# Optimization experiments

Hardware: AMD Instinct MI355X
Metric: run time of the kernel (lower is better)

Reference implementation:

```python
import jax, jax.numpy as jnp
import numpy as np

N_ATOMS = 4096
N_EDGES = 131072
NUM_BASIS = 8
CUTOFF = 6.0
EMBED = 64      # atom embedding dim
HID = 128       # hidden channel width
SH_DIM = 9      # l=0,1,2 spherical harmonics
TP_IN = HID * SH_DIM  # 1152
N_HEADS = 4
HEAD_DIM = HID // N_HEADS


def _spherical_harmonics(vec):
    # vec: [E,3] -> [E,9] matching the torch SphericalHarmonics (l=0,1,2)
    r = jnp.linalg.norm(vec, axis=-1, keepdims=True) + 1e-8
    u = vec / r
    x, y, z = u[:, 0], u[:, 1], u[:, 2]
    l0 = jnp.ones_like(x)[:, None]
    l1 = jnp.stack([y, z, x], axis=-1)
    l2 = jnp.stack([3.0 * z * z - 1.0, x * z, y * z, x * y, x * x - y * y], axis=-1)
    return jnp.concatenate([l0, l1, l2], axis=-1)


def _rbf(d):
    # bessel RBF with cosine cutoff, d: [E] -> [E, NUM_BASIS]
    freqs = jnp.arange(1, NUM_BASIS + 1, dtype=d.dtype) * (np.pi / CUTOFF)
    cut = 0.5 * (jnp.cos(d * (np.pi / CUTOFF)) + 1.0) * (d < CUTOFF).astype(d.dtype)
    rbf = jnp.sin(d[:, None] * freqs) / d[:, None]
    return rbf * cut[:, None]


def _mace_block(atomic_numbers, edge_index, edge_vectors, edge_lengths,
                atom_embed, rad_w1, rad_b1, rad_w2, rad_b2, tp_w, tp_b,
                msg_w1, msg_b1, msg_w2, msg_b2,
                attn_w_in, attn_b_in, attn_w_out, attn_b_out,
                gate_w, gate_b, out_w, out_b):
    n_atoms = atom_embed.shape[0] if False else atomic_numbers.shape[0]
    node = atom_embed[atomic_numbers]                      # [N,64] gather
    sh = _spherical_harmonics(edge_vectors)                # [E,9]
    rbf = _rbf(edge_lengths)                               # [E,8]
    rad = jax.nn.silu(rbf @ rad_w1 + rad_b1)
    rad = jax.nn.silu(rad @ rad_w2 + rad_b2)               # [E,128]
    # per-l outer products radial x sh_l, flattened channel-major, concatenated
    slices = [(0, 1), (1, 4), (4, 9)]
    msgs = jnp.concatenate(
        [(rad[:, :, None] * sh[:, None, s:e]).reshape(rad.shape[0], -1) for s, e in slices],
        axis=-1)                                           # [E,1152]
    edge_msg = msgs @ tp_w + tp_b                          # [E,128]
    dst = edge_index[1]
    agg = jax.ops.segment_sum(edge_msg, dst, num_segments=n_atoms)  # [N,128] scatter-add
    combined = jnp.concatenate([node, agg], axis=-1)       # [N,192]
    upd = jax.nn.silu(combined @ msg_w1 + msg_b1) @ msg_w2 + msg_b2  # [N,128]
    # multi-head self-attention over all atoms (batch of 1)
    qkv = upd @ attn_w_in.T + attn_b_in                    # [N,384]
    q, k, v = jnp.split(qkv, 3, axis=-1)
    q = q.reshape(-1, N_HEADS, HEAD_DIM)
    k = k.reshape(-1, N_HEADS, HEAD_DIM)
    v = v.reshape(-1, N_HEADS, HEAD_DIM)
    scores = jnp.einsum('nhd,mhd->hnm', q, k) / np.sqrt(HEAD_DIM)
    attn = jax.nn.softmax(scores, axis=-1)
    att = jnp.einsum('hnm,mhd->nhd', attn, v).reshape(-1, HID)
    att = att @ attn_w_out.T + attn_b_out                  # [N,128]
    gate = jax.nn.sigmoid(upd @ gate_w + gate_b)
    out = gate * att + (1.0 - gate) * upd
    return out @ out_w + out_b                             # [N,128]


def setup_inputs() -> dict:
    key = jax.random.key(0)
    ks = jax.random.split(key, 20)
    def w(k, shape, s=0.05):
        return jax.random.normal(k, shape, dtype=jnp.float32) * s
    return {
        'atomic_numbers': jax.random.randint(ks[0], (N_ATOMS,), 0, 100),
        'positions': jax.random.normal(ks[1], (N_ATOMS, 3), dtype=jnp.float32),
        'edge_index': jax.random.randint(ks[2], (2, N_EDGES), 0, N_ATOMS),
        'edge_vectors': jax.random.normal(ks[3], (N_EDGES, 3), dtype=jnp.float32),
        'edge_lengths': jax.random.uniform(ks[4], (N_EDGES,), dtype=jnp.float32, minval=0.5, maxval=5.9),
        'atom_embed': w(ks[5], (100, EMBED), 1.0),
        'rad_w1': w(ks[6], (NUM_BASIS, 64)), 'rad_b1': jnp.zeros((64,), jnp.float32),
        'rad_w2': w(ks[7], (64, HID)), 'rad_b2': jnp.zeros((HID,), jnp.float32),
        'tp_w': w(ks[8], (TP_IN, HID)), 'tp_b': jnp.zeros((HID,), jnp.float32),
        'msg_w1': w(ks[9], (EMBED + HID, HID)), 'msg_b1': jnp.zeros((HID,), jnp.float32),
        'msg_w2': w(ks[10], (HID, HID)), 'msg_b2': jnp.zeros((HID,), jnp.float32),
        'attn_w_in': w(ks[11], (3 * HID, HID)), 'attn_b_in': jnp.zeros((3 * HID,), jnp.float32),
        'attn_w_out': w(ks[12], (HID, HID)), 'attn_b_out': jnp.zeros((HID,), jnp.float32),
        'gate_w': w(ks[13], (HID, HID)), 'gate_b': jnp.zeros((HID,), jnp.float32),
        'out_w': w(ks[14], (HID, HID)), 'out_b': jnp.zeros((HID,), jnp.float32),
    }


def reference(atomic_numbers, positions, edge_index, edge_vectors, edge_lengths,
              atom_embed, rad_w1, rad_b1, rad_w2, rad_b2, tp_w, tp_b,
              msg_w1, msg_b1, msg_w2, msg_b2,
              attn_w_in, attn_b_in, attn_w_out, attn_b_out,
              gate_w, gate_b, out_w, out_b):
    # positions is accepted (as in the torch signature) but unused by the block math
    del positions
    return _mace_block(atomic_numbers, edge_index, edge_vectors, edge_lengths,
                       atom_embed, rad_w1, rad_b1, rad_w2, rad_b2, tp_w, tp_b,
                       msg_w1, msg_b1, msg_w2, msg_b2,
                       attn_w_in, attn_b_in, attn_w_out, attn_b_out,
                       gate_w, gate_b, out_w, out_b)
```

## Files before the change

kernel.cpp:

```cpp
#include <hip/hip_runtime.h>
#include <math.h>

#define N_ATOMS 4096
#define N_EDGES 131072
#define PI6 0.52359877559829887f
#define CAP 128

typedef __attribute__((ext_vector_type(8))) short bf16x8;
typedef __attribute__((ext_vector_type(4))) float f32x4;

#define MFMA(A,B,C) __builtin_amdgcn_mfma_f32_16x16x32_bf16((A),(B),(C),0,0,0)

__device__ __forceinline__ float silu_f(float x){ return x / (1.f + __expf(-x)); }
__device__ __forceinline__ float sigmoid_f(float x){ return 1.f / (1.f + __expf(-x)); }
__device__ __forceinline__ unsigned int f2bf(float f){
  unsigned int u = __float_as_uint(f);
  return (u + 0x7FFFu + ((u>>16)&1u)) >> 16;
}
__device__ __forceinline__ bf16x8 ld8(const unsigned short* p){
  union { unsigned int u[4]; bf16x8 v; } r;
  const unsigned int* q = (const unsigned int*)p;
  r.u[0]=q[0]; r.u[1]=q[1]; r.u[2]=q[2]; r.u[3]=q[3];
  return r.v;
}
__device__ __forceinline__ void split_store(float v, unsigned short* ph, unsigned short* pl){
  unsigned int hb = f2bf(v);
  *ph = (unsigned short)hb;
  *pl = (unsigned short)f2bf(v - __uint_as_float(hb<<16));
}

__global__ __launch_bounds__(256) void prep_kernel(
  const float* __restrict__ attn_w_out, const float* __restrict__ rad_w2,
  const float* __restrict__ tp_w, const float* __restrict__ msg_w1,
  const float* __restrict__ msg_w2, const float* __restrict__ attn_w_in,
  float* __restrict__ wt_out, int* __restrict__ cursor,
  unsigned short* __restrict__ w2t_h, unsigned short* __restrict__ w2t_l,
  unsigned short* __restrict__ tpwT_h, unsigned short* __restrict__ tpwT_l,
  unsigned short* __restrict__ w1T_h, unsigned short* __restrict__ w1T_l,
  unsigned short* __restrict__ w2T_h, unsigned short* __restrict__ w2T_l,
  unsigned short* __restrict__ awin_h, unsigned short* __restrict__ awin_l)
{
  int idx = blockIdx.x*256 + threadIdx.x;
  if (idx < 4096) cursor[idx] = 0;
  if (idx < 16384){
    int i = idx>>7, k = idx&127;
    wt_out[k*128+i] = attn_w_out[idx];
  } else if (idx < 24576){
    int j = idx - 16384; int k = j>>7, c = j&127;
    split_store(rad_w2[k*128+c], &w2t_h[c*64+k], &w2t_l[c*64+k]);
  } else if (idx < 172032){
    int j = idx - 24576; int col = j&127, kk = j>>7;
    int jj = kk>>7, c = kk&127;
    int r = (jj==0)? c : (jj<4 ? 128 + c*3 + (jj-1) : 512 + c*5 + (jj-4));
    split_store(tp_w[r*128+col], &tpwT_h[col*1152+kk], &tpwT_l[col*1152+kk]);
  } else if (idx < 196608){
    int j = idx - 172032; int col = j&127, k = j>>7;
    split_store(msg_w1[k*128+col], &w1T_h[col*192+k], &w1T_l[col*192+k]);
  } else if (idx < 212992){
    int j = idx - 196608; int col = j&127, k = j>>7;
    split_store(msg_w2[k*128+col], &w2T_h[col*128+k], &w2T_l[col*128+k]);
  } else if (idx < 262144){
    int j = idx - 212992;
    split_store(attn_w_in[j], &awin_h[j], &awin_l[j]);
  }
}

__global__ __launch_bounds__(256) void bucket_kernel(
  const int* __restrict__ edge_index, int* __restrict__ cursor, int* __restrict__ edge_slot)
{
  int e = blockIdx.x*256 + threadIdx.x;
  if (e < N_EDGES){
    int d = edge_index[N_EDGES + e];
    int pos = atomicAdd(&cursor[d], 1);
    if (pos < CAP) edge_slot[d*CAP + pos] = e;
  }
}

__global__ __launch_bounds__(512) void edge_F_kernel(
  const float* __restrict__ edge_vectors, const float* __restrict__ edge_lengths,
  const float* __restrict__ rad_w1, const float* __restrict__ rad_b1,
  const unsigned short* __restrict__ w2t_h, const unsigned short* __restrict__ w2t_l,
  const float* __restrict__ rad_b2,
  const int* __restrict__ cursor, const int* __restrict__ edge_slot,
  unsigned short* __restrict__ Fh, unsigned short* __restrict__ Fl)
{
  const int tid = threadIdx.x;
  const int w = tid >> 6, lane = tid & 63;
  const int l15 = lane & 15, lg = lane >> 4;
  const int m = w >> 1, nh = w & 1;

  __shared__ unsigned short W1h[64][36],  W1l[64][36];
  __shared__ unsigned short RBh[64][36],  RBl[64][36];
  __shared__ unsigned short SHh[16][72],  SHl[16][72];
  __shared__ unsigned short R1h[64][66],  R1l[64][66];
  __shared__ unsigned short R2wh[8][16][34], R2wl[8][16][34];

  bf16x8 WAh[2], WAl[2];
  {
    int c = w*16 + l15;
    WAh[0] = ld8(&w2t_h[c*64 + lg*8]);
    WAh[1] = ld8(&w2t_h[c*64 + 32 + lg*8]);
    WAl[0] = ld8(&w2t_l[c*64 + lg*8]);
    WAl[1] = ld8(&w2t_l[c*64 + 32 + lg*8]);
  }

  for (int i = tid; i < 64*36; i += 512){
    int c = i/36, k = i%36;
    float v = (k < 8) ? rad_w1[k*64 + c] : 0.f;
    split_store(v, &W1h[c][k], &W1l[c][k]);
    RBh[c][k]=0; RBl[c][k]=0;
  }
  for (int i = tid; i < 16*72; i += 512){ SHh[i/72][i%72]=0; SHl[i/72][i%72]=0; }

  const float b1A = rad_b1[nh*32 + l15];
  const float b1B = rad_b1[nh*32 + 16 + l15];
  float b2r[4];
  #pragma unroll
  for (int r=0;r<4;r++) b2r[r] = rad_b2[w*16 + lg*4 + r];

  __syncthreads();

  for (int aa = 0; aa < 4; ++aa){
    const int a = blockIdx.x*4 + aa;
    const int deg = min(cursor[a], CAP);
    const int base = a*CAP;
    f32x4 facc = {0.f,0.f,0.f,0.f};

    for (int t0 = 0; t0 < deg; t0 += 64){
      {
        int e8 = tid >> 3, u = tid & 7;
        int idx = t0 + e8;
        bool val = idx < deg;
        int eid = edge_slot[base + (val ? idx : 0)];
        float d = edge_lengths[eid];
        float cut = 0.5f*(__cosf(d*PI6)+1.f)*(d<6.f?1.f:0.f);
        float rb = __sinf(d*((float)(u+1)*PI6))/d*cut;
        split_store(rb, &RBh[e8][u], &RBl[e8][u]);
        float vx = edge_vectors[eid*3], vy = edge_vectors[eid*3+1], vz = edge_vectors[eid*3+2];
        float rn = sqrtf(vx*vx+vy*vy+vz*vz) + 1e-8f;
        float x = vx/rn, y = vy/rn, z = vz/rn;
        float sv;
        switch(u){
          case 0: sv = 1.f; break;
          case 1: sv = y; break;
          case 2: sv = z; break;
          case 3: sv = x; break;
          case 4: sv = 3.f*z*z-1.f; break;
          case 5: sv = x*z; break;
          case 6: sv = y*z; break;
          default: sv = x*y; break;
        }
        if (!val) sv = 0.f;
        split_store(sv, &SHh[u][e8], &SHl[u][e8]);
        if (u == 0){
          float s8 = val ? (x*x - y*y) : 0.f;
          split_store(s8, &SHh[8][e8], &SHl[8][e8]);
        }
      }
      __syncthreads();

      {
        bf16x8 Ah = ld8(&RBh[m*16 + l15][lg*8]);
        bf16x8 Al = ld8(&RBl[m*16 + l15][lg*8]);
        #pragma unroll
        for (int nt=0; nt<2; nt++){
          int c = nh*32 + nt*16 + l15;
          bf16x8 Bh = ld8(&W1h[c][lg*8]);
          bf16x8 Bl = ld8(&W1l[c][lg*8]);
          f32x4 z = {0.f,0.f,0.f,0.f};
          z = MFMA(Ah,Bl,z); z = MFMA(Al,Bh,z); z = MFMA(Ah,Bh,z);
          float bb = nt ? b1B : b1A;
          #pragma unroll
          for (int r=0;r<4;r++){
            int e8 = m*16 + lg*4 + r;
            int cc = nh*32 + nt*16 + l15;
            float v = silu_f(z[r] + bb);
            split_store(v, &R1h[e8][cc], &R1l[e8][cc]);
          }
        }
      }
      __syncthreads();

      #pragma unroll
      for (int eh=0; eh<2; eh++){
        #pragma unroll
        for (int nt2=0; nt2<2; nt2++){
          int et = eh*2 + nt2;
          bf16x8 Bh0 = ld8(&R1h[et*16+l15][lg*8]);
          bf16x8 Bh1 = ld8(&R1h[et*16+l15][32+lg*8]);
          bf16x8 Bl0 = ld8(&R1l[et*16+l15][lg*8]);
          bf16x8 Bl1 = ld8(&R1l[et*16+l15][32+lg*8]);
          f32x4 z = {0.f,0.f,0.f,0.f};
          z = MFMA(WAl[0],Bh0,z); z = MFMA(WAl[1],Bh1,z);
          z = MFMA(WAh[0],Bl0,z); z = MFMA(WAh[1],Bl1,z);
          z = MFMA(WAh[0],Bh0,z); z = MFMA(WAh[1],Bh1,z);
          #pragma unroll
          for (int r=0;r<4;r++){
            float v = silu_f(z[r] + b2r[r]);
            split_store(v, &R2wh[w][lg*4+r][nt2*16+l15], &R2wl[w][lg*4+r][nt2*16+l15]);
          }
        }
        __asm__ volatile("s_waitcnt lgkmcnt(0)" ::: "memory");
        {
          bf16x8 Ah = ld8(&R2wh[w][l15][lg*8]);
          bf16x8 Al = ld8(&R2wl[w][l15][lg*8]);
          bf16x8 Bh = ld8(&SHh[l15][eh*32 + lg*8]);
          bf16x8 Bl = ld8(&SHl[l15][eh*32 + lg*8]);
          facc = MFMA(Ah,Bl,facc);
          facc = MFMA(Al,Bh,facc);
          facc = MFMA(Ah,Bh,facc);
        }
      }
      __syncthreads();
    }

    if (l15 < 9){
      #pragma unroll
      for (int r=0;r<4;r++){
        int c = w*16 + lg*4 + r;
        size_t o = (size_t)l15*(N_ATOMS*128) + (size_t)a*128 + c;
        split_store(facc[r], &Fh[o], &Fl[o]);
      }
    }
  }
}

__global__ __launch_bounds__(512) void node_kernel(
  const int* __restrict__ atomic_numbers, const float* __restrict__ atom_embed,
  const unsigned short* __restrict__ Fh, const unsigned short* __restrict__ Fl,
  const unsigned short* __restrict__ tpwT_h, const unsigned short* __restrict__ tpwT_l,
  const float* __restrict__ tp_b, const int* __restrict__ cursor,
  const unsigned short* __restrict__ w1T_h, const unsigned short* __restrict__ w1T_l,
  const float* __restrict__ msg_b1,
  const unsigned short* __restrict__ w2T_h, const unsigned short* __restrict__ w2T_l,
  const float* __restrict__ msg_b2,
  const unsigned short* __restrict__ awin_h, const unsigned short* __restrict__ awin_l,
  const float* __restrict__ attn_b_in,
  float* __restrict__ upd_out,
  unsigned short* __restrict__ Qbf, unsigned short* __restrict__ Kbf,
  unsigned short* __restrict__ Vtb)
{
  const int a0 = blockIdx.x*16, tid = threadIdx.x;
  const int w = tid>>6, lane = tid&63, l15 = lane&15, lg = lane>>4;

  __shared__ unsigned short Ch[16][200], Cl[16][200];
  __shared__ unsigned short Hh[16][136], Hl[16][136];
  __shared__ unsigned short Uh[16][136], Ul[16][136];

  for (int i=tid; i<1024; i+=512){
    int a16=i>>6, k=i&63;
    float v = atom_embed[atomic_numbers[a0+a16]*64+k];
    split_store(v, &Ch[a16][k], &Cl[a16][k]);
  }

  {
    f32x4 z = {0.f,0.f,0.f,0.f};
    for (int ch=0; ch<36; ch++){
      int k0=ch*32, j=k0>>7, c0=k0&127;
      size_t aoff = (size_t)j*(N_ATOMS*128) + (size_t)(a0+l15)*128 + c0 + lg*8;
      bf16x8 Ah=ld8(Fh+aoff), Al=ld8(Fl+aoff);
      size_t boff = (size_t)(w*16+l15)*1152 + k0 + lg*8;
      bf16x8 Bh=ld8(tpwT_h+boff), Bl=ld8(tpwT_l+boff);
      z = MFMA(Ah,Bl,z); z = MFMA(Al,Bh,z); z = MFMA(Ah,Bh,z);
    }
    int col = w*16+l15;
    float tb = tp_b[col];
    #pragma unroll
    for (int r=0;r<4;r++){
      int row = lg*4+r, arow = a0+row;
      float deg = (float)cursor[arow];
      float v = z[r] + tb*deg;
      split_store(v, &Ch[row][64+col], &Cl[row][64+col]);
    }
  }
  __syncthreads();

  {
    f32x4 z = {0.f,0.f,0.f,0.f};
    #pragma unroll
    for (int ch=0; ch<6; ch++){
      int k0=ch*32;
      bf16x8 Ah=ld8(&Ch[l15][k0+lg*8]), Al=ld8(&Cl[l15][k0+lg*8]);
      size_t boff=(size_t)(w*16+l15)*192 + k0 + lg*8;
      bf16x8 Bh=ld8(w1T_h+boff), Bl=ld8(w1T_l+boff);
      z = MFMA(Ah,Bl,z); z = MFMA(Al,Bh,z); z = MFMA(Ah,Bh,z);
    }
    int col = w*16+l15;
    float mb = msg_b1[col];
    #pragma unroll
    for (int r=0;r<4;r++){
      int row = lg*4+r;
      float v = silu_f(z[r]+mb);
      split_store(v, &Hh[row][col], &Hl[row][col]);
    }
  }
  __syncthreads();

  {
    f32x4 z = {0.f,0.f,0.f,0.f};
    #pragma unroll
    for (int ch=0; ch<4; ch++){
      int k0=ch*32;
      bf16x8 Ah=ld8(&Hh[l15][k0+lg*8]), Al=ld8(&Hl[l15][k0+lg*8]);
      size_t boff=(size_t)(w*16+l15)*128 + k0 + lg*8;
      bf16x8 Bh=ld8(w2T_h+boff), Bl=ld8(w2T_l+boff);
      z = MFMA(Ah,Bl,z); z = MFMA(Al,Bh,z); z = MFMA(Ah,Bh,z);
    }
    int col = w*16+l15;
    float mb = msg_b2[col];
    #pragma unroll
    for (int r=0;r<4;r++){
      int row = lg*4+r;
      float v = z[r]+mb;
      upd_out[(size_t)(a0+row)*128 + col] = v;
      split_store(v, &Uh[row][col], &Ul[row][col]);
    }
  }
  __syncthreads();

  #pragma unroll
  for (int t3=0; t3<3; t3++){
    f32x4 z = {0.f,0.f,0.f,0.f};
    int col = (w*3+t3)*16 + l15;
    #pragma unroll
    for (int ch=0; ch<4; ch++){
      int k0=ch*32;
      bf16x8 Ah=ld8(&Uh[l15][k0+lg*8]), Al=ld8(&Ul[l15][k0+lg*8]);
      size_t boff=(size_t)col*128 + k0 + lg*8;
      bf16x8 Bh=ld8(awin_h+boff), Bl=ld8(awin_l+boff);
      z = MFMA(Ah,Bl,z); z = MFMA(Al,Bh,z); z = MFMA(Ah,Bh,z);
    }
    float ab = attn_b_in[col];
    int p = col>>7, hh = (col>>5)&3, dd = col&31;
    #pragma unroll
    for (int r=0;r<4;r++){
      int row = a0 + lg*4 + r;
      float v = z[r]+ab;
      if (p==0)      Qbf[(size_t)hh*131072 + (size_t)row*32 + dd] =
                       (unsigned short)f2bf(v*0.17677669529663687f);
      else if (p==1) Kbf[(size_t)hh*131072 + (size_t)row*32 + dd] = (unsigned short)f2bf(v);
      else           Vtb[(size_t)hh*131072 + (size_t)dd*4096 + row] = (unsigned short)f2bf(v);
    }
  }
}

__global__ __launch_bounds__(512) void attn_kernel(
  const unsigned short* __restrict__ Qbf, const unsigned short* __restrict__ Kbf,
  const unsigned short* __restrict__ Vtb, float* __restrict__ att)
{
  const int tid = threadIdx.x;
  const int w = tid>>6, lane = tid&63, l15 = lane&15, lg = lane>>4;
  const int qjl = w>>2, ks = w&3;
  const int qj = blockIdx.x*2 + qjl;
  const int h = qj >> 8, qt = qj & 255;

  __shared__ unsigned short Ps[8][16][72];
  __shared__ float MBo[2][4][16][32];
  __shared__ float MBm[2][4][16];
  __shared__ float MBs[2][4][16];

  const unsigned short* Kb = Kbf + (size_t)h*131072;
  const unsigned short* Vb = Vtb + (size_t)h*131072;

  bf16x8 bQ = ld8(&Qbf[(size_t)h*131072 + (size_t)(qt*16+l15)*32 + lg*8]);

  float m = -3e38f, su = 0.f;
  f32x4 oacc[2] = {{0.f,0.f,0.f,0.f},{0.f,0.f,0.f,0.f}};

  for (int kt = ks*16; kt < ks*16 + 16; ++kt){
    const int k0 = kt*64;
    f32x4 s[4];
    #pragma unroll
    for (int n=0;n<4;n++){
      bf16x8 aK = ld8(&Kb[(size_t)(k0+n*16+l15)*32 + lg*8]);
      f32x4 z = {0.f,0.f,0.f,0.f};
      s[n] = MFMA(aK, bQ, z);
    }
    float tmax = s[0][0];
    #pragma unroll
    for (int n=0;n<4;n++)
      #pragma unroll
      for (int r=0;r<4;r++) tmax = fmaxf(tmax, s[n][r]);
    tmax = fmaxf(tmax, __shfl_xor(tmax,16,64));
    tmax = fmaxf(tmax, __shfl_xor(tmax,32,64));
    float mn = fmaxf(m, tmax);
    float csc = __expf(m - mn);
    m = mn;
    float psum = 0.f;
    unsigned int* prow = (unsigned int*)&Ps[w][l15][0];
    #pragma unroll
    for (int n=0;n<4;n++){
      float p0=__expf(s[n][0]-mn), p1=__expf(s[n][1]-mn);
      float p2=__expf(s[n][2]-mn), p3=__expf(s[n][3]-mn);
      psum += (p0+p1)+(p2+p3);
      prow[n*8+lg*2]   = f2bf(p0) | (f2bf(p1)<<16);
      prow[n*8+lg*2+1] = f2bf(p2) | (f2bf(p3)<<16);
    }
    psum += __shfl_xor(psum,16,64);
    psum += __shfl_xor(psum,32,64);
    su = su*csc + psum;
    float cr[4];
    #pragma unroll
    for (int r=0;r<4;r++) cr[r] = __shfl(csc, lg*4+r, 64);
    #pragma unroll
    for (int nd=0;nd<2;nd++)
      #pragma unroll
      for (int r=0;r<4;r++) oacc[nd][r] *= cr[r];
    __asm__ volatile("s_waitcnt lgkmcnt(0)" ::: "memory");
    #pragma unroll
    for (int kc=0;kc<2;kc++){
      bf16x8 aP = ld8(&Ps[w][l15][kc*32 + lg*8]);
      #pragma unroll
      for (int nd=0;nd<2;nd++){
        bf16x8 bV = ld8(&Vb[(size_t)(nd*16+l15)*4096 + k0 + kc*32 + lg*8]);
        oacc[nd] = MFMA(aP, bV, oacc[nd]);
      }
    }
  }

  if (lg==0){ MBm[qjl][ks][l15]=m; MBs[qjl][ks][l15]=su; }
  #pragma unroll
  for (int nd=0;nd<2;nd++)
    #pragma unroll
    for (int r=0;r<4;r++) MBo[qjl][ks][lg*4+r][nd*16+l15] = oacc[nd][r];
  __syncthreads();

  for (int idx = tid; idx < 1024; idx += 512){
    int qq = idx>>9, q = (idx>>5)&15, d = idx&31;
    float m0=MBm[qq][0][q], m1=MBm[qq][1][q], m2=MBm[qq][2][q], m3=MBm[qq][3][q];
    float mf = fmaxf(fmaxf(m0,m1), fmaxf(m2,m3));
    float c0=__expf(m0-mf), c1=__expf(m1-mf), c2=__expf(m2-mf), c3=__expf(m3-mf);
    float st = MBs[qq][0][q]*c0 + MBs[qq][1][q]*c1 + MBs[qq][2][q]*c2 + MBs[qq][3][q]*c3;
    float o  = MBo[qq][0][q][d]*c0 + MBo[qq][1][q][d]*c1 + MBo[qq][2][q][d]*c2 + MBo[qq][3][q][d]*c3;
    int qj2 = blockIdx.x*2 + qq;
    int hh = qj2>>8, qrow = (qj2&255)*16 + q;
    att[(size_t)qrow*128 + hh*32 + d] = o/st;
  }
}

__global__ __launch_bounds__(512) void final_kernel(
  const float* __restrict__ att, const float* __restrict__ upd,
  const float* __restrict__ wt_out, const float* __restrict__ attn_b_out,
  const float* __restrict__ gate_w, const float* __restrict__ gate_b,
  const float* __restrict__ out_w, const float* __restrict__ out_b,
  float* __restrict__ out)
{
  const int a0 = blockIdx.x*8, tid = threadIdx.x;
  const int g = tid >> 7, o = tid & 127;
  __shared__ float att_s[8][128], upd_s[8][128], tmps[8][128];
  for (int i=tid; i<1024; i+=512){
    int a8 = i>>7, k = i&127;
    att_s[a8][k] = att[(a0+a8)*128+k];
    upd_s[a8][k] = upd[(a0+a8)*128+k];
  }
  __syncthreads();
  const int aA = 2*g, aB = 2*g+1;
  float a2A = attn_b_out[o], a2B = a2A;
  float gA = gate_b[o], gB = gA;
  for (int k=0;k<128;k++){
    float wa = wt_out[k*128+o];
    float wg = gate_w[k*128+o];
    a2A += att_s[aA][k]*wa; a2B += att_s[aB][k]*wa;
    gA  += upd_s[aA][k]*wg; gB  += upd_s[aB][k]*wg;
  }
  gA = sigmoid_f(gA); gB = sigmoid_f(gB);
  tmps[aA][o] = gA*a2A + (1.f-gA)*upd_s[aA][o];
  tmps[aB][o] = gB*a2B + (1.f-gB)*upd_s[aB][o];
  __syncthreads();
  float ouA = out_b[o], ouB = ouA;
  for (int k=0;k<128;k++){
    float w = out_w[k*128+o];
    ouA += tmps[aA][k]*w; ouB += tmps[aB][k]*w;
  }
  out[(a0+aA)*128+o] = ouA;
  out[(a0+aB)*128+o] = ouB;
}

extern "C" void kernel_launch(void* const* d_in, const int* in_sizes, int n_in,
                              void* d_out, int out_size, void* d_ws, size_t ws_size,
                              hipStream_t stream){
  const int*   atomic_numbers = (const int*)  d_in[0];
  const int*   edge_index     = (const int*)  d_in[2];
  const float* edge_vectors   = (const float*)d_in[3];
  const float* edge_lengths   = (const float*)d_in[4];
  const float* atom_embed     = (const float*)d_in[5];
  const float* rad_w1 = (const float*)d_in[6];
  const float* rad_b1 = (const float*)d_in[7];
  const float* rad_w2 = (const float*)d_in[8];
  const float* rad_b2 = (const float*)d_in[9];
  const float* tp_w   = (const float*)d_in[10];
  const float* tp_b   = (const float*)d_in[11];
  const float* msg_w1 = (const float*)d_in[12];
  const float* msg_b1 = (const float*)d_in[13];
  const float* msg_w2 = (const float*)d_in[14];
  const float* msg_b2 = (const float*)d_in[15];
  const float* attn_w_in  = (const float*)d_in[16];
  const float* attn_b_in  = (const float*)d_in[17];
  const float* attn_w_out = (const float*)d_in[18];
  const float* attn_b_out = (const float*)d_in[19];
  const float* gate_w = (const float*)d_in[20];
  const float* gate_b = (const float*)d_in[21];
  const float* out_w  = (const float*)d_in[22];
  const float* out_b  = (const float*)d_in[23];

  char* ws = (char*)d_ws;
  int* cursor    = (int*)(ws);
  int* edge_slot = (int*)(ws + 16384);
  float* wt_out  = (float*)(ws + 2113536);
  unsigned short* w2t_h  = (unsigned short*)(ws + 2179072);
  unsigned short* w2t_l  = (unsigned short*)(ws + 2195456);
  unsigned short* tpwT_h = (unsigned short*)(ws + 2211840);
  unsigned short* tpwT_l = (unsigned short*)(ws + 2506752);
  unsigned short* w1T_h  = (unsigned short*)(ws + 2801664);
  unsigned short* w1T_l  = (unsigned short*)(ws + 2850816);
  unsigned short* w2T_h  = (unsigned short*)(ws + 2899968);
  unsigned short* w2T_l  = (unsigned short*)(ws + 2932736);
  unsigned short* awin_h = (unsigned short*)(ws + 2965504);
  unsigned short* awin_l = (unsigned short*)(ws + 3063808);
  unsigned short* Fbf_h  = (unsigned short*)(ws + 3162112);
  unsigned short* Fbf_l  = (unsigned short*)(ws + 12599296);
  float* att     = (float*)(ws + 3162112);
  float* upd     = (float*)(ws + 22036480);
  unsigned short* Qbf = (unsigned short*)(ws + 24133632);
  unsigned short* Kbf = (unsigned short*)(ws + 25182208);
  unsigned short* Vtb = (unsigned short*)(ws + 26230784);

  prep_kernel<<<1024, 256, 0, stream>>>(attn_w_out, rad_w2, tp_w, msg_w1, msg_w2, attn_w_in,
      wt_out, cursor, w2t_h, w2t_l, tpwT_h, tpwT_l, w1T_h, w1T_l, w2T_h, w2T_l, awin_h, awin_l);
  bucket_kernel<<<(N_EDGES+255)/256, 256, 0, stream>>>(edge_index, cursor, edge_slot);
  edge_F_kernel<<<N_ATOMS/4, 512, 0, stream>>>(edge_vectors, edge_lengths,
      rad_w1, rad_b1, w2t_h, w2t_l, rad_b2, cursor, edge_slot, Fbf_h, Fbf_l);
  node_kernel<<<N_ATOMS/16, 512, 0, stream>>>(atomic_numbers, atom_embed,
      Fbf_h, Fbf_l, tpwT_h, tpwT_l, tp_b, cursor,
      w1T_h, w1T_l, msg_b1, w2T_h, w2T_l, msg_b2, awin_h, awin_l, attn_b_in,
      upd, Qbf, Kbf, Vtb);
  attn_kernel<<<512, 512, 0, stream>>>(Qbf, Kbf, Vtb, att);
  final_kernel<<<N_ATOMS/8, 512, 0, stream>>>(att, upd, wt_out, attn_b_out,
      gate_w, gate_b, out_w, out_b, (float*)d_out);
}
```

Before: 192.4 us.

## Restructure edge_F kernel to one atom per 256-thread block with 32-edge tiles

Changes the edge radial/feature kernel from 512-thread blocks that each loop over four atoms with 64-edge tiles to one atom per 256-thread block with 32-edge tiles. Each wave now covers two 16-channel output tiles, holding twice the rad_w2 fragments and two accumulators. The aim is to cut padding waste on low-degree atoms, since average degree is 32, and to raise block count and occupancy. The cost is more per-block setup (W1 staging and weight loads) across 4096 blocks and higher register use per thread.

```diff
diff --git a/kernel.cpp b/kernel.cpp
--- a/kernel.cpp
+++ b/kernel.cpp
@@ -76,7 +76,7 @@
   }
 }
 
-__global__ __launch_bounds__(512) void edge_F_kernel(
+__global__ __launch_bounds__(256) void edge_F_kernel(
   const float* __restrict__ edge_vectors, const float* __restrict__ edge_lengths,
   const float* __restrict__ rad_w1, const float* __restrict__ rad_b1,
   const unsigned short* __restrict__ w2t_h, const unsigned short* __restrict__ w2t_l,
@@ -84,57 +84,60 @@
   const int* __restrict__ cursor, const int* __restrict__ edge_slot,
   unsigned short* __restrict__ Fh, unsigned short* __restrict__ Fl)
 {
-  const int tid = threadIdx.x;
+  const int a = blockIdx.x, tid = threadIdx.x;
   const int w = tid >> 6, lane = tid & 63;
   const int l15 = lane & 15, lg = lane >> 4;
   const int m = w >> 1, nh = w & 1;
 
   __shared__ unsigned short W1h[64][36],  W1l[64][36];
-  __shared__ unsigned short RBh[64][36],  RBl[64][36];
-  __shared__ unsigned short SHh[16][72],  SHl[16][72];
-  __shared__ unsigned short R1h[64][66],  R1l[64][66];
-  __shared__ unsigned short R2wh[8][16][34], R2wl[8][16][34];
-
-  bf16x8 WAh[2], WAl[2];
-  {
-    int c = w*16 + l15;
-    WAh[0] = ld8(&w2t_h[c*64 + lg*8]);
-    WAh[1] = ld8(&w2t_h[c*64 + 32 + lg*8]);
-    WAl[0] = ld8(&w2t_l[c*64 + lg*8]);
-    WAl[1] = ld8(&w2t_l[c*64 + 32 + lg*8]);
-  }
-
-  for (int i = tid; i < 64*36; i += 512){
+  __shared__ unsigned short RBh[32][36],  RBl[32][36];
+  __shared__ unsigned short SHh[16][36],  SHl[16][36];
+  __shared__ unsigned short R1h[32][66],  R1l[32][66];
+  __shared__ unsigned short R2wh[4][2][16][34], R2wl[4][2][16][34];
+
+  bf16x8 WAh[2][2], WAl[2][2];
+  #pragma unroll
+  for (int ct=0; ct<2; ct++){
+    int c = (2*w+ct)*16 + l15;
+    WAh[ct][0] = ld8(&w2t_h[c*64 + lg*8]);
+    WAh[ct][1] = ld8(&w2t_h[c*64 + 32 + lg*8]);
+    WAl[ct][0] = ld8(&w2t_l[c*64 + lg*8]);
+    WAl[ct][1] = ld8(&w2t_l[c*64 + 32 + lg*8]);
+  }
+
+  for (int i = tid; i < 64*36; i += 256){
     int c = i/36, k = i%36;
     float v = (k < 8) ? rad_w1[k*64 + c] : 0.f;
     split_store(v, &W1h[c][k], &W1l[c][k]);
-    RBh[c][k]=0; RBl[c][k]=0;
-  }
-  for (int i = tid; i < 16*72; i += 512){ SHh[i/72][i%72]=0; SHl[i/72][i%72]=0; }
+  }
+  for (int i = tid; i < 32*36; i += 256){ RBh[i/36][i%36]=0; RBl[i/36][i%36]=0; }
+  for (int i = tid; i < 16*36; i += 256){ SHh[i/36][i%36]=0; SHl[i/36][i%36]=0; }
 
   const float b1A = rad_b1[nh*32 + l15];
   const float b1B = rad_b1[nh*32 + 16 + l15];
-  float b2r[4];
+  float b2r[2][4];
   #pragma unroll
-  for (int r=0;r<4;r++) b2r[r] = rad_b2[w*16 + lg*4 + r];
-
-  __syncthreads();
-
-  for (int aa = 0; aa < 4; ++aa){
-    const int a = blockIdx.x*4 + aa;
-    const int deg = min(cursor[a], CAP);
-    const int base = a*CAP;
-    f32x4 facc = {0.f,0.f,0.f,0.f};
-
-    for (int t0 = 0; t0 < deg; t0 += 64){
-      {
-        int e8 = tid >> 3, u = tid & 7;
+  for (int ct=0; ct<2; ct++)
+    #pragma unroll
+    for (int r=0;r<4;r++) b2r[ct][r] = rad_b2[(2*w+ct)*16 + lg*4 + r];
+
+  const int deg = min(cursor[a], CAP);
+  const int base = a*CAP;
+  f32x4 facc[2] = {{0.f,0.f,0.f,0.f},{0.f,0.f,0.f,0.f}};
+
+  __syncthreads();
+
+  for (int t0 = 0; t0 < deg; t0 += 32){
+    {
+      int e8 = tid >> 3, u = tid & 7;
+      if (t0 + (w<<3) < deg){
         int idx = t0 + e8;
         bool val = idx < deg;
         int eid = edge_slot[base + (val ? idx : 0)];
         float d = edge_lengths[eid];
         float cut = 0.5f*(__cosf(d*PI6)+1.f)*(d<6.f?1.f:0.f);
         float rb = __sinf(d*((float)(u+1)*PI6))/d*cut;
+        if (!val) rb = 0.f;
         split_store(rb, &RBh[e8][u], &RBl[e8][u]);
         float vx = edge_vectors[eid*3], vy = edge_vectors[eid*3+1], vz = edge_vectors[eid*3+2];
         float rn = sqrtf(vx*vx+vy*vy+vz*vz) + 1e-8f;
@@ -156,70 +159,75 @@
           float s8 = val ? (x*x - y*y) : 0.f;
           split_store(s8, &SHh[8][e8], &SHl[8][e8]);
         }
+      } else {
+        RBh[e8][u]=0; RBl[e8][u]=0;
+        SHh[u][e8]=0; SHl[u][e8]=0;
+        if (u==0){ SHh[8][e8]=0; SHl[8][e8]=0; }
       }
-      __syncthreads();
-
-      {
-        bf16x8 Ah = ld8(&RBh[m*16 + l15][lg*8]);
-        bf16x8 Al = ld8(&RBl[m*16 + l15][lg*8]);
+    }
+    __syncthreads();
+
+    {
+      bf16x8 Ah = ld8(&RBh[m*16 + l15][lg*8]);
+      bf16x8 Al = ld8(&RBl[m*16 + l15][lg*8]);
+      #pragma unroll
+      for (int nt=0; nt<2; nt++){
+        int c = nh*32 + nt*16 + l15;
+        bf16x8 Bh = ld8(&W1h[c][lg*8]);
+        bf16x8 Bl = ld8(&W1l[c][lg*8]);
+        f32x4 z = {0.f,0.f,0.f,0.f};
+        z = MFMA(Ah,Bl,z); z = MFMA(Al,Bh,z); z = MFMA(Ah,Bh,z);
+        float bb = nt ? b1B : b1A;
         #pragma unroll
-        for (int nt=0; nt<2; nt++){
-          int c = nh*32 + nt*16 + l15;
-          bf16x8 Bh = ld8(&W1h[c][lg*8]);
-          bf16x8 Bl = ld8(&W1l[c][lg*8]);
-          f32x4 z = {0.f,0.f,0.f,0.f};
-          z = MFMA(Ah,Bl,z); z = MFMA(Al,Bh,z); z = MFMA(Ah,Bh,z);
-          float bb = nt ? b1B : b1A;
-          #pragma unroll
-          for (int r=0;r<4;r++){
-            int e8 = m*16 + lg*4 + r;
-            int cc = nh*32 + nt*16 + l15;
-            float v = silu_f(z[r] + bb);
-            split_store(v, &R1h[e8][cc], &R1l[e8][cc]);
-          }
+        for (int r=0;r<4;r++){
+          int e8 = m*16 + lg*4 + r;
+          float v = silu_f(z[r] + bb);
+          split_store(v, &R1h[e8][c], &R1l[e8][c]);
         }
       }
-      __syncthreads();
-
+    }
+    __syncthreads();
+
+    #pragma unroll
+    for (int ct=0; ct<2; ct++){
       #pragma unroll
-      for (int eh=0; eh<2; eh++){
+      for (int et=0; et<2; et++){
+        bf16x8 Bh0 = ld8(&R1h[et*16+l15][lg*8]);
+        bf16x8 Bh1 = ld8(&R1h[et*16+l15][32+lg*8]);
+        bf16x8 Bl0 = ld8(&R1l[et*16+l15][lg*8]);
+        bf16x8 Bl1 = ld8(&R1l[et*16+l15][32+lg*8]);
+        f32x4 z = {0.f,0.f,0.f,0.f};
+        z = MFMA(WAl[ct][0],Bh0,z); z = MFMA(WAl[ct][1],Bh1,z);
+        z = MFMA(WAh[ct][0],Bl0,z); z = MFMA(WAh[ct][1],Bl1,z);
+        z = MFMA(WAh[ct][0],Bh0,z); z = MFMA(WAh[ct][1],Bh1,z);
         #pragma unroll
-        for (int nt2=0; nt2<2; nt2++){
-          int et = eh*2 + nt2;
-          bf16x8 Bh0 = ld8(&R1h[et*16+l15][lg*8]);
-          bf16x8 Bh1 = ld8(&R1h[et*16+l15][32+lg*8]);
-          bf16x8 Bl0 = ld8(&R1l[et*16+l15][lg*8]);
-          bf16x8 Bl1 = ld8(&R1l[et*16+l15][32+lg*8]);
-          f32x4 z = {0.f,0.f,0.f,0.f};
-          z = MFMA(WAl[0],Bh0,z); z = MFMA(WAl[1],Bh1,z);
-          z = MFMA(WAh[0],Bl0,z); z = MFMA(WAh[1],Bl1,z);
-          z = MFMA(WAh[0],Bh0,z); z = MFMA(WAh[1],Bh1,z);
-          #pragma unroll
-          for (int r=0;r<4;r++){
-            float v = silu_f(z[r] + b2r[r]);
-            split_store(v, &R2wh[w][lg*4+r][nt2*16+l15], &R2wl[w][lg*4+r][nt2*16+l15]);
-          }
-        }
-        __asm__ volatile("s_waitcnt lgkmcnt(0)" ::: "memory");
-        {
-          bf16x8 Ah = ld8(&R2wh[w][l15][lg*8]);
-          bf16x8 Al = ld8(&R2wl[w][l15][lg*8]);
-          bf16x8 Bh = ld8(&SHh[l15][eh*32 + lg*8]);
-          bf16x8 Bl = ld8(&SHl[l15][eh*32 + lg*8]);
-          facc = MFMA(Ah,Bl,facc);
-          facc = MFMA(Al,Bh,facc);
-          facc = MFMA(Ah,Bh,facc);
+        for (int r=0;r<4;r++){
+          float v = silu_f(z[r] + b2r[ct][r]);
+          split_store(v, &R2wh[w][ct][lg*4+r][et*16+l15], &R2wl[w][ct][lg*4+r][et*16+l15]);
         }
       }
-      __syncthreads();
-    }
-
-    if (l15 < 9){
+      __asm__ volatile("s_waitcnt lgkmcnt(0)" ::: "memory");
+      {
+        bf16x8 Ah = ld8(&R2wh[w][ct][l15][lg*8]);
+        bf16x8 Al = ld8(&R2wl[w][ct][l15][lg*8]);
+        bf16x8 Bh = ld8(&SHh[l15][lg*8]);
+        bf16x8 Bl = ld8(&SHl[l15][lg*8]);
+        facc[ct] = MFMA(Ah,Bl,facc[ct]);
+        facc[ct] = MFMA(Al,Bh,facc[ct]);
+        facc[ct] = MFMA(Ah,Bh,facc[ct]);
+      }
+    }
+    __syncthreads();
+  }
+
+  if (l15 < 9){
+    #pragma unroll
+    for (int ct=0; ct<2; ct++){
       #pragma unroll
       for (int r=0;r<4;r++){
-        int c = w*16 + lg*4 + r;
+        int c = (2*w+ct)*16 + lg*4 + r;
         size_t o = (size_t)l15*(N_ATOMS*128) + (size_t)a*128 + c;
-        split_store(facc[r], &Fh[o], &Fl[o]);
+        split_store(facc[ct][r], &Fh[o], &Fl[o]);
       }
     }
   }
@@ -528,7 +536,7 @@
   prep_kernel<<<1024, 256, 0, stream>>>(attn_w_out, rad_w2, tp_w, msg_w1, msg_w2, attn_w_in,
       wt_out, cursor, w2t_h, w2t_l, tpwT_h, tpwT_l, w1T_h, w1T_l, w2T_h, w2T_l, awin_h, awin_l);
   bucket_kernel<<<(N_EDGES+255)/256, 256, 0, stream>>>(edge_index, cursor, edge_slot);
-  edge_F_kernel<<<N_ATOMS/4, 512, 0, stream>>>(edge_vectors, edge_lengths,
+  edge_F_kernel<<<N_ATOMS, 256, 0, stream>>>(edge_vectors, edge_lengths,
       rad_w1, rad_b1, w2t_h, w2t_l, rad_b2, cursor, edge_slot, Fbf_h, Fbf_l);
   node_kernel<<<N_ATOMS/16, 512, 0, stream>>>(atomic_numbers, atom_embed,
       Fbf_h, Fbf_l, tpwT_h, tpwT_l, tp_b, cursor,
```

Result: slower. 199.4 us (+3.7%).
